# Optimization experiments

Hardware: AMD Instinct MI355X
Metric: run time of the kernel (lower is better)

The kernel has to match this reference:

```python
import jax, jax.numpy as jnp
import numpy as np

ALPHA = 0.1          # dt / tau = 10 / 100
HIDDEN_NOISE = 0.1   # std of per-step hidden noise


def setup_inputs() -> dict:
    key = jax.random.key(0)
    k1, k2, k3, k4, k5 = jax.random.split(key, 5)
    B, T, I, H, O = 128, 800, 9, 1024, 8
    x = jax.random.normal(k1, (B, T, I), dtype=jnp.float32)
    noise = jax.random.normal(k2, (B, T, H), dtype=jnp.float32)
    # xavier/kaiming-like scaled Gaussian init for the weight matrices
    Win = jax.random.normal(k3, (H, I), dtype=jnp.float32) * (1.0 / np.sqrt(I))
    Wrec = jax.random.normal(k4, (H, H), dtype=jnp.float32) * (1.0 / np.sqrt(H))
    Wout = jax.random.normal(k5, (O, H), dtype=jnp.float32) * (1.0 / np.sqrt(H))
    return {"x": x, "noise": noise, "Win": Win, "Wrec": Wrec, "Wout": Wout}


def reference(x, noise, Win, Wrec, Wout):
    # Precompute input drive for all timesteps: it + noise  -> [B, T, H]
    drive = jnp.einsum('bti,hi->bth', x, Win) + HIDDEN_NOISE * noise
    B = x.shape[0]
    H = Wrec.shape[0]
    h0 = jnp.zeros((B, H), dtype=x.dtype)

    def step(h, d):  # d: [B, H] drive at time t
        pre = d + h @ Wrec.T
        h_new = jax.nn.relu(pre) * ALPHA + (1.0 - ALPHA) * h
        return h_new, h_new

    _, hs = jax.lax.scan(step, h0, jnp.swapaxes(drive, 0, 1))  # hs: [T, B, H]
    hiddens = jnp.swapaxes(hs, 0, 1)                            # [B, T, H]
    logits = jnp.einsum('bth,oh->bto', hiddens, Wout)           # [B, T, O]
    outs = jax.nn.softmax(logits, axis=-1)
    return hiddens, outs
```

## Files before the change

### kernel.cpp

```cpp
#include <hip/hip_runtime.h>

#define B_TOT 128
#define T_LEN 800
#define I_DIM 9
#define H_DIM 1024
#define O_DIM 8
#define NB    16
#define NSLC  8
#define NCOL  128
#define GROUPS (B_TOT / NB)

typedef float f32x4 __attribute__((ext_vector_type(4)));
typedef short s16x8 __attribute__((ext_vector_type(8)));
typedef unsigned long long u64;

__device__ __forceinline__ unsigned short f2bf(float f) {
    unsigned u = __float_as_uint(f);
    u += 0x7fffu + ((u >> 16) & 1u);
    return (unsigned short)(u >> 16);
}

__global__ __launch_bounds__(512, 1)
void rnn_scan(const float* __restrict__ x,
              const float* __restrict__ noise,
              const float* __restrict__ Win,
              const float* __restrict__ Wrec,
              unsigned short* __restrict__ hx,
              unsigned* __restrict__ flags,
              float* __restrict__ hiddens)
{
    __shared__ char  hlds[NB * 2048];
    __shared__ float xs[NB][I_DIM];

    const int tid  = threadIdx.x;
    const int lane = tid & 63;
    const int w    = tid >> 6;
    const int g    = blockIdx.x & 7;
    const int s    = blockIdx.x >> 3;
    const int b0   = g * NB;
    const int l15  = lane & 15;
    const int kb   = lane >> 4;
    const int n    = s * NCOL + w * 16 + l15;

    s16x8 breg[32];
    {
        const float* wrow = Wrec + (size_t)n * H_DIM + kb * 8;
#pragma unroll
        for (int kt = 0; kt < 32; ++kt) {
            float4 v0 = *(const float4*)(wrow + kt * 32);
            float4 v1 = *(const float4*)(wrow + kt * 32 + 4);
            union { s16x8 v; unsigned short u[8]; } r;
            r.u[0] = f2bf(v0.x); r.u[1] = f2bf(v0.y); r.u[2] = f2bf(v0.z); r.u[3] = f2bf(v0.w);
            r.u[4] = f2bf(v1.x); r.u[5] = f2bf(v1.y); r.u[6] = f2bf(v1.z); r.u[7] = f2bf(v1.w);
            breg[kt] = r.v;
        }
    }

    float win[I_DIM];
#pragma unroll
    for (int i = 0; i < I_DIM; ++i) win[i] = Win[n * I_DIM + i];

    unsigned short* hxg     = hx + (size_t)g * (2 * NB * H_DIM);
    unsigned*       myflags = flags + g * (NSLC * 32);

    const int grow = 2 * w + (lane >> 5);
    const int gbc  = (lane & 31) * 64;

    float hreg[4] = {0.f, 0.f, 0.f, 0.f};

#pragma unroll 1
    for (int t = 0; t < T_LEN; ++t) {
        if (tid < NB * I_DIM) {
            int b = tid / I_DIM, i = tid - b * I_DIM;
            xs[b][i] = x[((size_t)(b0 + b) * T_LEN + t) * I_DIM + i];
        }
        float nz[4];
#pragma unroll
        for (int r = 0; r < 4; ++r)
            nz[r] = noise[((size_t)(b0 + kb * 4 + r) * T_LEN + t) * H_DIM + n];

        if (t > 0) {
            if (w == 0) {
                const unsigned tgt = (unsigned)t;
                unsigned f;
                do {
                    f = (lane < NSLC)
                        ? __hip_atomic_load(myflags + lane * 32, __ATOMIC_RELAXED,
                                            __HIP_MEMORY_SCOPE_AGENT)
                        : tgt;
                } while (__any(f < tgt));
            }
            __syncthreads();
            asm volatile("" ::: "memory");

            const char* srcrow = (const char*)(hxg + ((t - 1) & 1) * (NB * H_DIM))
                                 + grow * 2048 + gbc;
            u64 v[8];
#pragma unroll
            for (int j = 0; j < 8; ++j)
                v[j] = __hip_atomic_load((const u64*)srcrow + j, __ATOMIC_RELAXED,
                                         __HIP_MEMORY_SCOPE_AGENT);
            char* drow = hlds + grow * 2048;
#pragma unroll
            for (int j = 0; j < 4; ++j) {
                ulonglong2 q; q.x = v[2 * j]; q.y = v[2 * j + 1];
                *(ulonglong2*)(drow + ((gbc + j * 16) ^ ((grow & 7) << 4))) = q;
            }
            __syncthreads();
        } else {
            __syncthreads();
        }

        f32x4 acc = {0.f, 0.f, 0.f, 0.f};
        if (t > 0) {
#pragma unroll
            for (int kt = 0; kt < 32; ++kt) {
                s16x8 af = *(const s16x8*)(hlds + l15 * 2048 +
                                           ((kt * 64 + kb * 16) ^ ((l15 & 7) << 4)));
                acc = __builtin_amdgcn_mfma_f32_16x16x32_bf16(af, breg[kt], acc, 0, 0, 0);
            }
        }

#pragma unroll
        for (int r = 0; r < 4; ++r) {
            const int b = kb * 4 + r;
            float d = 0.1f * nz[r];
#pragma unroll
            for (int i = 0; i < I_DIM; ++i) d += win[i] * xs[b][i];
            const float pre = acc[r] + d;
            hreg[r] = 0.9f * hreg[r] + 0.1f * fmaxf(pre, 0.f);
        }

        unsigned* hdst32 = (unsigned*)(hxg + (t & 1) * (NB * H_DIM));
#pragma unroll
        for (int r = 0; r < 4; ++r) {
            unsigned self  = f2bf(hreg[r]);
            unsigned other = __shfl_xor(self, 1, 64);
            if (!(l15 & 1))
                __hip_atomic_store(hdst32 + (kb * 4 + r) * (H_DIM / 2) + (n >> 1),
                                   self | (other << 16), __ATOMIC_RELAXED,
                                   __HIP_MEMORY_SCOPE_AGENT);
        }
        asm volatile("s_waitcnt vmcnt(0)" ::: "memory");
        __syncthreads();
        if (tid == 0)
            __hip_atomic_store(myflags + s * 32, (unsigned)(t + 1),
                               __ATOMIC_RELAXED, __HIP_MEMORY_SCOPE_AGENT);

#pragma unroll
        for (int r = 0; r < 4; ++r)
            __builtin_nontemporal_store(
                hreg[r], &hiddens[((size_t)(b0 + kb * 4 + r) * T_LEN + t) * H_DIM + n]);
    }
}

__global__ __launch_bounds__(256)
void out_head(const float* __restrict__ hiddens, const float* __restrict__ Wout,
              float* __restrict__ outs)
{
    __shared__ float wlds[O_DIM][H_DIM];
    const int tid = threadIdx.x;
    for (int j = tid; j < (O_DIM * H_DIM) / 4; j += 256)
        ((float4*)wlds)[j] = ((const float4*)Wout)[j];
    __syncthreads();

    const int wave = tid >> 6, lane = tid & 63;
#pragma unroll
    for (int rr = 0; rr < 2; ++rr) {
        const size_t row = (size_t)blockIdx.x * 8 + wave * 2 + rr;
        const float* hp = hiddens + row * H_DIM;

        float a0=0,a1=0,a2=0,a3=0,a4=0,a5=0,a6=0,a7=0;
#pragma unroll
        for (int j = 0; j < 4; ++j) {
            float4 hv = *(const float4*)(hp + lane * 4 + j * 256);
#define DOT(o, acc) { float4 wv = *(const float4*)&wlds[o][lane*4 + j*256]; \
                      acc += hv.x*wv.x + hv.y*wv.y + hv.z*wv.z + hv.w*wv.w; }
            DOT(0,a0) DOT(1,a1) DOT(2,a2) DOT(3,a3)
            DOT(4,a4) DOT(5,a5) DOT(6,a6) DOT(7,a7)
#undef DOT
        }
#pragma unroll
        for (int off = 32; off; off >>= 1) {
            a0 += __shfl_xor(a0, off, 64); a1 += __shfl_xor(a1, off, 64);
            a2 += __shfl_xor(a2, off, 64); a3 += __shfl_xor(a3, off, 64);
            a4 += __shfl_xor(a4, off, 64); a5 += __shfl_xor(a5, off, 64);
            a6 += __shfl_xor(a6, off, 64); a7 += __shfl_xor(a7, off, 64);
        }
        if (lane == 0) {
            float mx = fmaxf(fmaxf(fmaxf(a0,a1),fmaxf(a2,a3)),
                             fmaxf(fmaxf(a4,a5),fmaxf(a6,a7)));
            float e0=expf(a0-mx), e1=expf(a1-mx), e2=expf(a2-mx), e3=expf(a3-mx);
            float e4=expf(a4-mx), e5=expf(a5-mx), e6=expf(a6-mx), e7=expf(a7-mx);
            float inv = 1.f / (e0+e1+e2+e3+e4+e5+e6+e7);
            float* op = outs + row * O_DIM;
            op[0]=e0*inv; op[1]=e1*inv; op[2]=e2*inv; op[3]=e3*inv;
            op[4]=e4*inv; op[5]=e5*inv; op[6]=e6*inv; op[7]=e7*inv;
        }
    }
}

extern "C" void kernel_launch(void* const* d_in, const int* in_sizes, int n_in,
                              void* d_out, int out_size, void* d_ws, size_t ws_size,
                              hipStream_t stream) {
    const float* x     = (const float*)d_in[0];
    const float* noise = (const float*)d_in[1];
    const float* Win   = (const float*)d_in[2];
    const float* Wrec  = (const float*)d_in[3];
    const float* Wout  = (const float*)d_in[4];

    float* hiddens = (float*)d_out;
    float* outs    = hiddens + (size_t)B_TOT * T_LEN * H_DIM;

    unsigned*       flags = (unsigned*)d_ws;
    unsigned short* hx    = (unsigned short*)((char*)d_ws + 8192);

    hipMemsetAsync(d_ws, 0, 8192, stream);
    rnn_scan<<<GROUPS * NSLC, 512, 0, stream>>>(x, noise, Win, Wrec, hx, flags, hiddens);
    out_head<<<(B_TOT * T_LEN) / 8, 256, 0, stream>>>(hiddens, Wout, outs);
}
```

Baseline: 3.756 ms.

## Replace block barriers and LDS staging with per-wave flags and pipelined direct loads

Each wave now publishes its own completion flag instead of one flag per block. Consumers poll all 64 flags of the group with a ballot and wait only for the 128-column chunk they need next. The recurrent state is loaded from global memory straight into MFMA operand registers, with loads double-buffered against the MFMAs, so the LDS copy and both __syncthreads per step are gone. The input projection is computed per lane from global x rather than staged through shared memory. Because there is no block-level barrier, correctness now depends on ordering the per-wave flags, and the code issues more global atomic polling traffic.

```diff
diff --git a/kernel.cpp b/kernel.cpp
--- a/kernel.cpp
+++ b/kernel.cpp
@@ -20,7 +20,15 @@
     return (unsigned short)(u >> 16);
 }
 
-__global__ __launch_bounds__(512, 1)
+__device__ __forceinline__ s16x8 mk(u64 lo, u64 hi) {
+    union { u64 q[2]; s16x8 v; } u;
+    u.q[0] = lo; u.q[1] = hi;
+    return u.v;
+}
+
+#define AL(p) __hip_atomic_load((p), __ATOMIC_RELAXED, __HIP_MEMORY_SCOPE_AGENT)
+
+__global__ __launch_bounds__(512, 2)
 void rnn_scan(const float* __restrict__ x,
               const float* __restrict__ noise,
               const float* __restrict__ Win,
@@ -29,9 +37,6 @@
               unsigned* __restrict__ flags,
               float* __restrict__ hiddens)
 {
-    __shared__ char  hlds[NB * 2048];
-    __shared__ float xs[NB][I_DIM];
-
     const int tid  = threadIdx.x;
     const int lane = tid & 63;
     const int w    = tid >> 6;
@@ -61,75 +66,78 @@
     for (int i = 0; i < I_DIM; ++i) win[i] = Win[n * I_DIM + i];
 
     unsigned short* hxg     = hx + (size_t)g * (2 * NB * H_DIM);
-    unsigned*       myflags = flags + g * (NSLC * 32);
-
-    const int grow = 2 * w + (lane >> 5);
-    const int gbc  = (lane & 31) * 64;
+    unsigned*       gflags  = flags + g * 512;
+    const unsigned* fl      = gflags + lane * 8;
+    unsigned*       myflag  = gflags + (s * 8 + w) * 8;
 
     float hreg[4] = {0.f, 0.f, 0.f, 0.f};
 
 #pragma unroll 1
     for (int t = 0; t < T_LEN; ++t) {
-        if (tid < NB * I_DIM) {
-            int b = tid / I_DIM, i = tid - b * I_DIM;
-            xs[b][i] = x[((size_t)(b0 + b) * T_LEN + t) * I_DIM + i];
-        }
-        float nz[4];
+        float xd[4], nz[4];
+#pragma unroll
+        for (int r = 0; r < 4; ++r) {
+            const float* xp = x + ((size_t)(b0 + kb * 4 + r) * T_LEN + t) * I_DIM;
+            float sx = 0.f;
+#pragma unroll
+            for (int i = 0; i < I_DIM; ++i) sx += win[i] * xp[i];
+            xd[r] = sx;
+            nz[r] = noise[((size_t)(b0 + kb * 4 + r) * T_LEN + t) * H_DIM + n];
+        }
+
+        f32x4 acc0 = {0.f, 0.f, 0.f, 0.f}, acc1 = {0.f, 0.f, 0.f, 0.f};
+
+        if (t > 0) {
+            const unsigned tt = (unsigned)t;
+            u64 rdy = 0;
+            const u64* hq = (const u64*)(hxg + ((t - 1) & 1) * (NB * H_DIM))
+                            + l15 * 256 + kb * 2;
+
+#define WAITQ(q)                                                              \
+            while (((rdy >> ((q) * 8)) & 0xFFull) != 0xFFull) {               \
+                unsigned fv = AL(fl);                                         \
+                rdy = __ballot(fv >= tt);                                     \
+            }                                                                 \
+            asm volatile("" ::: "memory");
+
+#define ISSUE(A, q)                                                           \
+            A[0] = AL(hq + ((q) * 4 + 0) * 8); A[1] = AL(hq + ((q) * 4 + 0) * 8 + 1); \
+            A[2] = AL(hq + ((q) * 4 + 1) * 8); A[3] = AL(hq + ((q) * 4 + 1) * 8 + 1); \
+            A[4] = AL(hq + ((q) * 4 + 2) * 8); A[5] = AL(hq + ((q) * 4 + 2) * 8 + 1); \
+            A[6] = AL(hq + ((q) * 4 + 3) * 8); A[7] = AL(hq + ((q) * 4 + 3) * 8 + 1);
+
+#define MF(A, q)                                                              \
+            acc0 = __builtin_amdgcn_mfma_f32_16x16x32_bf16(mk(A[0], A[1]), breg[(q) * 4 + 0], acc0, 0, 0, 0); \
+            acc1 = __builtin_amdgcn_mfma_f32_16x16x32_bf16(mk(A[2], A[3]), breg[(q) * 4 + 1], acc1, 0, 0, 0); \
+            acc0 = __builtin_amdgcn_mfma_f32_16x16x32_bf16(mk(A[4], A[5]), breg[(q) * 4 + 2], acc0, 0, 0, 0); \
+            acc1 = __builtin_amdgcn_mfma_f32_16x16x32_bf16(mk(A[6], A[7]), breg[(q) * 4 + 3], acc1, 0, 0, 0);
+
+            u64 A0[8], A1[8];
+            WAITQ(0) ISSUE(A0, 0)
+            WAITQ(1) ISSUE(A1, 1) MF(A0, 0)
+            WAITQ(2) ISSUE(A0, 2) MF(A1, 1)
+            WAITQ(3) ISSUE(A1, 3) MF(A0, 2)
+            WAITQ(4) ISSUE(A0, 4) MF(A1, 3)
+            WAITQ(5) ISSUE(A1, 5) MF(A0, 4)
+            WAITQ(6) ISSUE(A0, 6) MF(A1, 5)
+            WAITQ(7) ISSUE(A1, 7) MF(A0, 6)
+            MF(A1, 7)
+#undef WAITQ
+#undef ISSUE
+#undef MF
+        }
+
+        const f32x4 acc = acc0 + acc1;
+#pragma unroll
+        for (int r = 0; r < 4; ++r) {
+            const float pre = acc[r] + xd[r] + 0.1f * nz[r];
+            hreg[r] = 0.9f * hreg[r] + 0.1f * fmaxf(pre, 0.f);
+        }
+
 #pragma unroll
         for (int r = 0; r < 4; ++r)
-            nz[r] = noise[((size_t)(b0 + kb * 4 + r) * T_LEN + t) * H_DIM + n];
-
-        if (t > 0) {
-            if (w == 0) {
-                const unsigned tgt = (unsigned)t;
-                unsigned f;
-                do {
-                    f = (lane < NSLC)
-                        ? __hip_atomic_load(myflags + lane * 32, __ATOMIC_RELAXED,
-                                            __HIP_MEMORY_SCOPE_AGENT)
-                        : tgt;
-                } while (__any(f < tgt));
-            }
-            __syncthreads();
-            asm volatile("" ::: "memory");
-
-            const char* srcrow = (const char*)(hxg + ((t - 1) & 1) * (NB * H_DIM))
-                                 + grow * 2048 + gbc;
-            u64 v[8];
-#pragma unroll
-            for (int j = 0; j < 8; ++j)
-                v[j] = __hip_atomic_load((const u64*)srcrow + j, __ATOMIC_RELAXED,
-                                         __HIP_MEMORY_SCOPE_AGENT);
-            char* drow = hlds + grow * 2048;
-#pragma unroll
-            for (int j = 0; j < 4; ++j) {
-                ulonglong2 q; q.x = v[2 * j]; q.y = v[2 * j + 1];
-                *(ulonglong2*)(drow + ((gbc + j * 16) ^ ((grow & 7) << 4))) = q;
-            }
-            __syncthreads();
-        } else {
-            __syncthreads();
-        }
-
-        f32x4 acc = {0.f, 0.f, 0.f, 0.f};
-        if (t > 0) {
-#pragma unroll
-            for (int kt = 0; kt < 32; ++kt) {
-                s16x8 af = *(const s16x8*)(hlds + l15 * 2048 +
-                                           ((kt * 64 + kb * 16) ^ ((l15 & 7) << 4)));
-                acc = __builtin_amdgcn_mfma_f32_16x16x32_bf16(af, breg[kt], acc, 0, 0, 0);
-            }
-        }
-
-#pragma unroll
-        for (int r = 0; r < 4; ++r) {
-            const int b = kb * 4 + r;
-            float d = 0.1f * nz[r];
-#pragma unroll
-            for (int i = 0; i < I_DIM; ++i) d += win[i] * xs[b][i];
-            const float pre = acc[r] + d;
-            hreg[r] = 0.9f * hreg[r] + 0.1f * fmaxf(pre, 0.f);
-        }
+            __builtin_nontemporal_store(
+                hreg[r], &hiddens[((size_t)(b0 + kb * 4 + r) * T_LEN + t) * H_DIM + n]);
 
         unsigned* hdst32 = (unsigned*)(hxg + (t & 1) * (NB * H_DIM));
 #pragma unroll
@@ -142,15 +150,9 @@
                                    __HIP_MEMORY_SCOPE_AGENT);
         }
         asm volatile("s_waitcnt vmcnt(0)" ::: "memory");
-        __syncthreads();
-        if (tid == 0)
-            __hip_atomic_store(myflags + s * 32, (unsigned)(t + 1),
-                               __ATOMIC_RELAXED, __HIP_MEMORY_SCOPE_AGENT);
-
-#pragma unroll
-        for (int r = 0; r < 4; ++r)
-            __builtin_nontemporal_store(
-                hreg[r], &hiddens[((size_t)(b0 + kb * 4 + r) * T_LEN + t) * H_DIM + n]);
+        if (lane == 0)
+            __hip_atomic_store(myflag, (unsigned)(t + 1), __ATOMIC_RELAXED,
+                               __HIP_MEMORY_SCOPE_AGENT);
     }
 }
 
@@ -213,9 +215,9 @@
     float* outs    = hiddens + (size_t)B_TOT * T_LEN * H_DIM;
 
     unsigned*       flags = (unsigned*)d_ws;
-    unsigned short* hx    = (unsigned short*)((char*)d_ws + 8192);
-
-    hipMemsetAsync(d_ws, 0, 8192, stream);
+    unsigned short* hx    = (unsigned short*)((char*)d_ws + 16384);
+
+    hipMemsetAsync(d_ws, 0, 16384, stream);
     rnn_scan<<<GROUPS * NSLC, 512, 0, stream>>>(x, noise, Win, Wrec, hx, flags, hiddens);
     out_head<<<(B_TOT * T_LEN) / 8, 256, 0, stream>>>(hiddens, Wout, outs);
 }
```

Result: slower. 14.45 ms (+284.7%).

## Replace flag handshake with tag bits embedded in exchanged bf16 hidden state

Applied to the files above, without the earlier changes.

The separate per-slice flag array, its spin loop, the vmcnt wait and the extra barriers are removed. Each step's bf16 hidden values now carry a parity tag in the sign bit, which is free because the hidden state is non-negative. Consumers spin directly on the data until the tags match, then mask them off. LDS staging and the x buffer are double-buffered so only one barrier remains per step. The MFMA chain is split into two accumulators, and the workspace is initialised to 0xFF so the initial tags read as invalid.

```diff
diff --git a/kernel.cpp b/kernel.cpp
--- a/kernel.cpp
+++ b/kernel.cpp
@@ -14,23 +14,31 @@
 typedef short s16x8 __attribute__((ext_vector_type(8)));
 typedef unsigned long long u64;
 
+#define TAGM 0x0000800000008000ull
+
 __device__ __forceinline__ unsigned short f2bf(float f) {
     unsigned u = __float_as_uint(f);
     u += 0x7fffu + ((u >> 16) & 1u);
     return (unsigned short)(u >> 16);
 }
 
-__global__ __launch_bounds__(512, 1)
+#define AL(p) __hip_atomic_load((p), __ATOMIC_RELAXED, __HIP_MEMORY_SCOPE_AGENT)
+#define AS(p, v) __hip_atomic_store((p), (v), __ATOMIC_RELAXED, __HIP_MEMORY_SCOPE_AGENT)
+
+__device__ __forceinline__ int swz(int s, int r) {
+    return s ^ ((s >> 3) & 7) ^ (r & 7);
+}
+
+__global__ __launch_bounds__(512, 2)
 void rnn_scan(const float* __restrict__ x,
               const float* __restrict__ noise,
               const float* __restrict__ Win,
               const float* __restrict__ Wrec,
               unsigned short* __restrict__ hx,
-              unsigned* __restrict__ flags,
               float* __restrict__ hiddens)
 {
-    __shared__ char  hlds[NB * 2048];
-    __shared__ float xs[NB][I_DIM];
+    __shared__ char  hlds[2][NB * 2048];
+    __shared__ float xs[2][NB][I_DIM];
 
     const int tid  = threadIdx.x;
     const int lane = tid & 63;
@@ -60,19 +68,28 @@
 #pragma unroll
     for (int i = 0; i < I_DIM; ++i) win[i] = Win[n * I_DIM + i];
 
-    unsigned short* hxg     = hx + (size_t)g * (2 * NB * H_DIM);
-    unsigned*       myflags = flags + g * (NSLC * 32);
+    unsigned short* hxg = hx + (size_t)g * (2 * NB * H_DIM);
 
     const int grow = 2 * w + (lane >> 5);
-    const int gbc  = (lane & 31) * 64;
+    const int gl   = lane & 31;
 
     float hreg[4] = {0.f, 0.f, 0.f, 0.f};
 
 #pragma unroll 1
     for (int t = 0; t < T_LEN; ++t) {
+        const int pb = t & 1;
+
+        u64 v[8];
+        const u64* src = (const u64*)(hxg + ((t - 1) & 1) * (NB * H_DIM))
+                         + grow * 256 + gl * 8;
+        if (t > 0) {
+#pragma unroll
+            for (int j = 0; j < 8; ++j) v[j] = AL(src + j);
+        }
+
         if (tid < NB * I_DIM) {
             int b = tid / I_DIM, i = tid - b * I_DIM;
-            xs[b][i] = x[((size_t)(b0 + b) * T_LEN + t) * I_DIM + i];
+            xs[pb][b][i] = x[((size_t)(b0 + b) * T_LEN + t) * I_DIM + i];
         }
         float nz[4];
 #pragma unroll
@@ -80,73 +97,64 @@
             nz[r] = noise[((size_t)(b0 + kb * 4 + r) * T_LEN + t) * H_DIM + n];
 
         if (t > 0) {
-            if (w == 0) {
-                const unsigned tgt = (unsigned)t;
-                unsigned f;
-                do {
-                    f = (lane < NSLC)
-                        ? __hip_atomic_load(myflags + lane * 32, __ATOMIC_RELAXED,
-                                            __HIP_MEMORY_SCOPE_AGENT)
-                        : tgt;
-                } while (__any(f < tgt));
+            const u64 exp = (((t - 1) >> 1) & 1) ? TAGM : 0ull;
+            for (;;) {
+                u64 bad = 0;
+#pragma unroll
+                for (int j = 0; j < 8; ++j) bad |= (v[j] ^ exp) & TAGM;
+                if (__all(bad == 0)) break;
+#pragma unroll
+                for (int j = 0; j < 8; ++j) v[j] = AL(src + j);
             }
-            __syncthreads();
-            asm volatile("" ::: "memory");
-
-            const char* srcrow = (const char*)(hxg + ((t - 1) & 1) * (NB * H_DIM))
-                                 + grow * 2048 + gbc;
-            u64 v[8];
-#pragma unroll
-            for (int j = 0; j < 8; ++j)
-                v[j] = __hip_atomic_load((const u64*)srcrow + j, __ATOMIC_RELAXED,
-                                         __HIP_MEMORY_SCOPE_AGENT);
-            char* drow = hlds + grow * 2048;
-#pragma unroll
-            for (int j = 0; j < 4; ++j) {
-                ulonglong2 q; q.x = v[2 * j]; q.y = v[2 * j + 1];
-                *(ulonglong2*)(drow + ((gbc + j * 16) ^ ((grow & 7) << 4))) = q;
+            char* drow = hlds[pb] + grow * 2048;
+#pragma unroll
+            for (int j2 = 0; j2 < 4; ++j2) {
+                ulonglong2 q;
+                q.x = v[2 * j2] & ~TAGM;
+                q.y = v[2 * j2 + 1] & ~TAGM;
+                *(ulonglong2*)(drow + swz(gl * 4 + j2, grow) * 16) = q;
             }
-            __syncthreads();
-        } else {
-            __syncthreads();
-        }
-
-        f32x4 acc = {0.f, 0.f, 0.f, 0.f};
+        }
+        __syncthreads();
+
+        float xd[4];
+#pragma unroll
+        for (int r = 0; r < 4; ++r) {
+            float sx = 0.f;
+#pragma unroll
+            for (int i = 0; i < I_DIM; ++i) sx += win[i] * xs[pb][kb * 4 + r][i];
+            xd[r] = sx;
+        }
+
+        f32x4 acc0 = {0.f, 0.f, 0.f, 0.f}, acc1 = {0.f, 0.f, 0.f, 0.f};
         if (t > 0) {
-#pragma unroll
-            for (int kt = 0; kt < 32; ++kt) {
-                s16x8 af = *(const s16x8*)(hlds + l15 * 2048 +
-                                           ((kt * 64 + kb * 16) ^ ((l15 & 7) << 4)));
-                acc = __builtin_amdgcn_mfma_f32_16x16x32_bf16(af, breg[kt], acc, 0, 0, 0);
+            const char* rrow = hlds[pb] + l15 * 2048;
+#pragma unroll
+            for (int kt = 0; kt < 32; kt += 2) {
+                s16x8 a0 = *(const s16x8*)(rrow + swz(kt * 4 + kb, l15) * 16);
+                acc0 = __builtin_amdgcn_mfma_f32_16x16x32_bf16(a0, breg[kt], acc0, 0, 0, 0);
+                s16x8 a1 = *(const s16x8*)(rrow + swz(kt * 4 + 4 + kb, l15) * 16);
+                acc1 = __builtin_amdgcn_mfma_f32_16x16x32_bf16(a1, breg[kt + 1], acc1, 0, 0, 0);
             }
         }
+        const f32x4 acc = acc0 + acc1;
 
 #pragma unroll
         for (int r = 0; r < 4; ++r) {
-            const int b = kb * 4 + r;
-            float d = 0.1f * nz[r];
-#pragma unroll
-            for (int i = 0; i < I_DIM; ++i) d += win[i] * xs[b][i];
-            const float pre = acc[r] + d;
+            const float pre = acc[r] + xd[r] + 0.1f * nz[r];
             hreg[r] = 0.9f * hreg[r] + 0.1f * fmaxf(pre, 0.f);
         }
 
-        unsigned* hdst32 = (unsigned*)(hxg + (t & 1) * (NB * H_DIM));
+        const unsigned tagbit = (unsigned)((t >> 1) & 1) << 15;
+        unsigned* hdst32 = (unsigned*)(hxg + pb * (NB * H_DIM));
 #pragma unroll
         for (int r = 0; r < 4; ++r) {
             unsigned self  = f2bf(hreg[r]);
             unsigned other = __shfl_xor(self, 1, 64);
             if (!(l15 & 1))
-                __hip_atomic_store(hdst32 + (kb * 4 + r) * (H_DIM / 2) + (n >> 1),
-                                   self | (other << 16), __ATOMIC_RELAXED,
-                                   __HIP_MEMORY_SCOPE_AGENT);
-        }
-        asm volatile("s_waitcnt vmcnt(0)" ::: "memory");
-        __syncthreads();
-        if (tid == 0)
-            __hip_atomic_store(myflags + s * 32, (unsigned)(t + 1),
-                               __ATOMIC_RELAXED, __HIP_MEMORY_SCOPE_AGENT);
-
+                AS(hdst32 + (kb * 4 + r) * (H_DIM / 2) + (n >> 1),
+                   self | (other << 16) | tagbit);
+        }
 #pragma unroll
         for (int r = 0; r < 4; ++r)
             __builtin_nontemporal_store(
@@ -212,10 +220,9 @@
     float* hiddens = (float*)d_out;
     float* outs    = hiddens + (size_t)B_TOT * T_LEN * H_DIM;
 
-    unsigned*       flags = (unsigned*)d_ws;
-    unsigned short* hx    = (unsigned short*)((char*)d_ws + 8192);
-
-    hipMemsetAsync(d_ws, 0, 8192, stream);
-    rnn_scan<<<GROUPS * NSLC, 512, 0, stream>>>(x, noise, Win, Wrec, hx, flags, hiddens);
+    unsigned short* hx = (unsigned short*)d_ws;
+
+    hipMemsetAsync(d_ws, 0xFF, (size_t)GROUPS * 2 * NB * H_DIM * 2, stream);
+    rnn_scan<<<GROUPS * NSLC, 512, 0, stream>>>(x, noise, Win, Wrec, hx, hiddens);
     out_head<<<(B_TOT * T_LEN) / 8, 256, 0, stream>>>(hiddens, Wout, outs);
 }
```

After: 6.835 ms. 1.82x slower.
